# Optimization experiments

Hardware: AMD Instinct MI355X
Metric: run time of the kernel (lower is better)

Reference implementation:

```python
import jax, jax.numpy as jnp
import numpy as np

EPS = 1e-8

def setup_inputs() -> dict:
    key = jax.random.key(0)
    k = jax.random.split(key, 5)
    b, cin, cout, hw, kh = 8, 128, 128, 256, 3
    cond = 128
    return {
        "x": jax.random.normal(k[0], (b, cin, hw, hw), jnp.float32),
        "y": jax.random.normal(k[1], (b, cond), jnp.float32),
        "conv_w": jax.random.normal(k[2], (cout, cin, kh, kh), jnp.float32) * 0.05,
        "gamma_w": jax.random.normal(k[3], (cin, cond), jnp.float32) * 0.05,
        "gamma_b": jnp.zeros((cin,), jnp.float32),
    }

def reference(x, y, conv_w, gamma_w, gamma_b):
    # x: [b, cin, h, w]; y: [b, cond]; conv_w: [cout, cin, kh, kw]
    b, c, h, w = x.shape
    cout = conv_w.shape[0]
    gamma = y @ gamma_w.T + gamma_b                                   # [b, cin]  (fc_gamma)
    weight = conv_w[None] * (gamma[:, None, :, None, None] + 1.0)     # [b, cout, cin, kh, kw]
    # demodulation: rsqrt of sum of squares over (cin, kh, kw)
    d = jax.lax.rsqrt(jnp.sum(weight * weight, axis=(2, 3, 4), keepdims=True) + EPS)
    weight = weight * d
    # grouped conv with groups = batch
    xg = x.reshape(1, b * c, h, w)
    wg = weight.reshape(b * cout, c, conv_w.shape[2], conv_w.shape[3])
    out = jax.lax.conv_general_dilated(
        xg, wg, window_strides=(1, 1), padding="SAME",
        dimension_numbers=("NCHW", "OIHW", "NCHW"),
        feature_group_count=b)
    return out.reshape(b, cout, h, w)
```

## Files before the change

### kernel.cpp

```cpp
#include <hip/hip_runtime.h>

typedef _Float16 f16;
typedef _Float16 f16x8 __attribute__((ext_vector_type(8)));
typedef float f32x4 __attribute__((ext_vector_type(4)));

#define NB 8
#define NC 128
#define HW 256
#define EPSV 1e-8f

__global__ __launch_bounds__(256) void k_weights(
    const float* __restrict__ y, const float* __restrict__ conv_w,
    const float* __restrict__ gamma_w, const float* __restrict__ gamma_b,
    f16* __restrict__ W16)
{
    int b  = blockIdx.x >> 7;
    int co = blockIdx.x & 127;
    int t  = threadIdx.x;

    __shared__ float g1[128];
    __shared__ float part[256];
    __shared__ float red[256];

    {
        int ci = t & 127, hf = t >> 7;
        const float* yb = y + b * 128 + hf * 64;
        const float* gw = gamma_w + (size_t)ci * 128 + hf * 64;
        float s = 0.f;
        #pragma unroll 8
        for (int j = 0; j < 64; ++j) s += yb[j] * gw[j];
        part[t] = s;
    }
    __syncthreads();
    if (t < 128) g1[t] = part[t] + part[t + 128] + gamma_b[t] + 1.0f;
    __syncthreads();

    const float* wrow = conv_w + (size_t)co * 1152;
    float ssq = 0.f;
    for (int i = t; i < 1152; i += 256) {
        int ci = i / 9;
        float wv = wrow[i] * g1[ci];
        ssq += wv * wv;
    }
    red[t] = ssq;
    __syncthreads();
    for (int s = 128; s > 0; s >>= 1) {
        if (t < s) red[t] += red[t + s];
        __syncthreads();
    }
    float d = rsqrtf(red[0] + EPSV);

    for (int i = t; i < 1152; i += 256) {
        int ci = i / 9, tap = i - ci * 9;
        float wv = wrow[i] * g1[ci] * d;
        int chunk = ci >> 5, ci_in = ci & 31;
        size_t wi = (((size_t)((b * 9 + tap) * 4 + chunk) * 128 + co) << 5) + ci_in;
        W16[wi] = (f16)wv;
    }
}

__global__ __launch_bounds__(256) void k_transpose(
    const float* __restrict__ x, f16* __restrict__ x16)
{
    int b = blockIdx.x >> 8;
    int y = blockIdx.x & 255;
    int l = threadIdx.x;

    const float* src = x + ((size_t)b * 128 * 65536) + (size_t)y * 256 + l;

    for (int c0 = 0; c0 < 128; c0 += 8) {
        uint u[4];
        #pragma unroll
        for (int i = 0; i < 8; i += 2) {
            float v0 = src[(size_t)(c0 + i) * 65536];
            float v1 = src[(size_t)(c0 + i + 1) * 65536];
            f16 h0 = (f16)v0, h1 = (f16)v1;
            ushort u0 = *(ushort*)&h0, u1 = *(ushort*)&h1;
            u[i >> 1] = (uint)u0 | ((uint)u1 << 16);
        }
        int chunk = c0 >> 5, ci_in = c0 & 31;
        f16* dst = x16 + (((size_t)(b * 4 + chunk) * 65536 + (size_t)y * 256 + l) << 5) + ci_in;
        *(uint4*)dst = *(uint4*)u;
    }
}

__device__ __forceinline__ uint4 load_xs_g(const f16* xc, int idx, int y0, int x0)
{
    int r = idx / 72;
    int rem = idx - r * 72;
    int yy = y0 + r - 1;
    int xx = x0 + (rem >> 2) - 1;
    if ((unsigned)yy < 256u && (unsigned)xx < 256u)
        return *(const uint4*)(xc + ((((size_t)yy << 8) + xx) << 5) + ((rem & 3) << 3));
    return make_uint4(0u, 0u, 0u, 0u);
}

__global__ __launch_bounds__(256) void k_conv(
    const f16* __restrict__ x16, const f16* __restrict__ W16,
    float* __restrict__ out)
{
    int blk  = blockIdx.x;
    int tile = blk & 511;
    int b    = blk >> 9;
    int tc   = tile & 15, tr = tile >> 4;
    int y0   = tr * 8, x0 = tc * 16;

    __shared__ f16 As[2][128 * 40];
    __shared__ f16 Xs[2][180 * 32];

    int t    = threadIdx.x;
    int w    = t >> 6, lane = t & 63;
    int wm   = (w >> 1) * 64;
    int wn   = (w & 1) * 4;
    int l15  = lane & 15;
    int k8   = lane >> 4;

    const f16* Wb = W16 + (size_t)b * 147456;

    {
        const f16* xc = x16 + (size_t)(b * 4) * 2097152;
        for (int idx = t; idx < 720; idx += 256) {
            uint4 v = load_xs_g(xc, idx, y0, x0);
            *(uint4*)((char*)(&Xs[0][0]) + (size_t)idx * 16) = v;
        }
        const uint4* asrc = (const uint4*)Wb;
        uint4* adst = (uint4*)((char*)(&As[0][0]) + (t >> 1) * 80 + (t & 1) * 32);
        adst[0] = asrc[(t >> 1) * 4 + (t & 1) * 2];
        adst[1] = asrc[(t >> 1) * 4 + (t & 1) * 2 + 1];
    }
    __syncthreads();

    f32x4 acc[4][4];
    #pragma unroll
    for (int mi = 0; mi < 4; ++mi)
        #pragma unroll
        for (int nj = 0; nj < 4; ++nj)
            acc[mi][nj] = (f32x4){0.f, 0.f, 0.f, 0.f};

    int chunk = 0, tap = 0;
    for (int it = 0; it < 36; ++it) {
        bool preA = it < 35;
        bool preX = (tap == 0) && (chunk < 3);

        uint4 a0 = {}, a1 = {};
        if (preA) {
            int tn = tap + 1, cn = chunk;
            if (tn == 9) { tn = 0; cn = chunk + 1; }
            const uint4* asrc = (const uint4*)(Wb + (size_t)(tn * 4 + cn) * 4096);
            a0 = asrc[(t >> 1) * 4 + (t & 1) * 2];
            a1 = asrc[(t >> 1) * 4 + (t & 1) * 2 + 1];
        }
        uint4 xv0 = {}, xv1 = {}, xv2 = {};
        if (preX) {
            const f16* xc = x16 + (size_t)(b * 4 + chunk + 1) * 2097152;
            xv0 = load_xs_g(xc, t, y0, x0);
            xv1 = load_xs_g(xc, t + 256, y0, x0);
            if (t < 208) xv2 = load_xs_g(xc, t + 512, y0, x0);
        }

        int dy = tap / 3, dx = tap - dy * 3;
        const f16* Ab = &As[it & 1][0];
        const f16* Xb = &Xs[chunk & 1][0];

        f16x8 af[4];
        #pragma unroll
        for (int mi = 0; mi < 4; ++mi)
            af[mi] = *(const f16x8*)(Ab + (wm + mi * 16 + l15) * 40 + k8 * 8);

        f16x8 bf[4];
        #pragma unroll
        for (int nj = 0; nj < 4; ++nj) {
            int p = (wn + nj + dy) * 18 + dx + l15;
            bf[nj] = *(const f16x8*)(Xb + p * 32 + k8 * 8);
        }

        #pragma unroll
        for (int mi = 0; mi < 4; ++mi)
            #pragma unroll
            for (int nj = 0; nj < 4; ++nj)
                acc[mi][nj] = __builtin_amdgcn_mfma_f32_16x16x32_f16(
                    af[mi], bf[nj], acc[mi][nj], 0, 0, 0);

        if (preA) {
            uint4* adst = (uint4*)((char*)(&As[(it + 1) & 1][0]) + (t >> 1) * 80 + (t & 1) * 32);
            adst[0] = a0; adst[1] = a1;
        }
        if (preX) {
            char* xd = (char*)(&Xs[(chunk + 1) & 1][0]);
            *(uint4*)(xd + (size_t)t * 16) = xv0;
            *(uint4*)(xd + (size_t)(t + 256) * 16) = xv1;
            if (t < 208) *(uint4*)(xd + (size_t)(t + 512) * 16) = xv2;
        }
        __syncthreads();

        if (++tap == 9) { tap = 0; ++chunk; }
    }

    size_t obase = (size_t)b << 23;
    #pragma unroll
    for (int mi = 0; mi < 4; ++mi) {
        #pragma unroll
        for (int r = 0; r < 4; ++r) {
            int co = wm + mi * 16 + k8 * 4 + r;
            float* orow = out + obase + ((size_t)co << 16);
            #pragma unroll
            for (int nj = 0; nj < 4; ++nj) {
                int yy = y0 + wn + nj;
                orow[(size_t)yy * 256 + x0 + l15] = acc[mi][nj][r];
            }
        }
    }
}

extern "C" void kernel_launch(void* const* d_in, const int* in_sizes, int n_in,
                              void* d_out, int out_size, void* d_ws, size_t ws_size,
                              hipStream_t stream)
{
    const float* x       = (const float*)d_in[0];
    const float* y       = (const float*)d_in[1];
    const float* conv_w  = (const float*)d_in[2];
    const float* gamma_w = (const float*)d_in[3];
    const float* gamma_b = (const float*)d_in[4];
    float* out = (float*)d_out;

    f16* x16 = (f16*)d_ws;
    f16* W16 = (f16*)((char*)d_ws + 134217728ull);

    k_weights<<<dim3(1024), dim3(256), 0, stream>>>(y, conv_w, gamma_w, gamma_b, W16);
    k_transpose<<<dim3(2048), dim3(256), 0, stream>>>(x, x16);
    k_conv<<<dim3(4096), dim3(256), 0, stream>>>(x16, W16, out);
}
```

Before: 671.9 us.

## Fuse fp32-to-fp16 input conversion into conv kernel, drop transpose pass

Removes the separate transpose kernel that converted x to a channel-interleaved fp16 buffer, and instead has the conv kernel load fp32 NCHW data directly, convert to fp16 and pack into shared memory. It also changes shared-memory pitches to 72 bytes for both A and X tiles, likely to reduce bank conflicts. This saves a full write and re-read of a 128MB intermediate. In exchange, each tile's global loads become strided scalar fp32 reads (8 channels at 256KB stride), halo data is re-read across tiles, and more registers are held during prefetch.

```diff
diff --git a/kernel.cpp b/kernel.cpp
--- a/kernel.cpp
+++ b/kernel.cpp
@@ -8,6 +8,9 @@
 #define NC 128
 #define HW 256
 #define EPSV 1e-8f
+
+#define APITCH 72
+#define XPITCH 72
 
 __global__ __launch_bounds__(256) void k_weights(
     const float* __restrict__ y, const float* __restrict__ conv_w,
@@ -59,44 +62,41 @@
     }
 }
 
-__global__ __launch_bounds__(256) void k_transpose(
-    const float* __restrict__ x, f16* __restrict__ x16)
-{
-    int b = blockIdx.x >> 8;
-    int y = blockIdx.x & 255;
-    int l = threadIdx.x;
-
-    const float* src = x + ((size_t)b * 128 * 65536) + (size_t)y * 256 + l;
-
-    for (int c0 = 0; c0 < 128; c0 += 8) {
-        uint u[4];
-        #pragma unroll
-        for (int i = 0; i < 8; i += 2) {
-            float v0 = src[(size_t)(c0 + i) * 65536];
-            float v1 = src[(size_t)(c0 + i + 1) * 65536];
-            f16 h0 = (f16)v0, h1 = (f16)v1;
-            ushort u0 = *(ushort*)&h0, u1 = *(ushort*)&h1;
-            u[i >> 1] = (uint)u0 | ((uint)u1 << 16);
-        }
-        int chunk = c0 >> 5, ci_in = c0 & 31;
-        f16* dst = x16 + (((size_t)(b * 4 + chunk) * 65536 + (size_t)y * 256 + l) << 5) + ci_in;
-        *(uint4*)dst = *(uint4*)u;
-    }
-}
-
-__device__ __forceinline__ uint4 load_xs_g(const f16* xc, int idx, int y0, int x0)
-{
-    int r = idx / 72;
+
+__device__ __forceinline__ void load8(float* __restrict__ v,
+                                      const float* __restrict__ xb,
+                                      int idx, int y0, int x0)
+{
+    int r   = idx / 72;
     int rem = idx - r * 72;
-    int yy = y0 + r - 1;
-    int xx = x0 + (rem >> 2) - 1;
-    if ((unsigned)yy < 256u && (unsigned)xx < 256u)
-        return *(const uint4*)(xc + ((((size_t)yy << 8) + xx) << 5) + ((rem & 3) << 3));
-    return make_uint4(0u, 0u, 0u, 0u);
+    int yy  = y0 + r - 1;
+    int xx  = x0 + (rem >> 2) - 1;
+    if (((unsigned)yy < 256u) & ((unsigned)xx < 256u)) {
+        const float* p = xb + (((size_t)(rem & 3)) << 19) + ((yy << 8) + xx);
+        #pragma unroll
+        for (int j = 0; j < 8; ++j) v[j] = p[(size_t)j << 16];
+    } else {
+        #pragma unroll
+        for (int j = 0; j < 8; ++j) v[j] = 0.f;
+    }
+}
+
+__device__ __forceinline__ void pack_write(char* __restrict__ xdst, int idx,
+                                           const float* __restrict__ v)
+{
+    uint u[4];
+    #pragma unroll
+    for (int j = 0; j < 8; j += 2) {
+        f16 h0 = (f16)v[j], h1 = (f16)v[j + 1];
+        ushort u0 = *(const ushort*)&h0, u1 = *(const ushort*)&h1;
+        u[j >> 1] = (uint)u0 | ((uint)u1 << 16);
+    }
+    int p = idx >> 2, g = idx & 3;
+    *(uint4*)(xdst + p * XPITCH + g * 16) = *(uint4*)u;
 }
 
 __global__ __launch_bounds__(256) void k_conv(
-    const f16* __restrict__ x16, const f16* __restrict__ W16,
+    const float* __restrict__ x, const f16* __restrict__ W16,
     float* __restrict__ out)
 {
     int blk  = blockIdx.x;
@@ -105,8 +105,8 @@
     int tc   = tile & 15, tr = tile >> 4;
     int y0   = tr * 8, x0 = tc * 16;
 
-    __shared__ f16 As[2][128 * 40];
-    __shared__ f16 Xs[2][180 * 32];
+    __shared__ char As[2][128 * APITCH];
+    __shared__ char Xs[2][180 * XPITCH];
 
     int t    = threadIdx.x;
     int w    = t >> 6, lane = t & 63;
@@ -118,13 +118,14 @@
     const f16* Wb = W16 + (size_t)b * 147456;
 
     {
-        const f16* xc = x16 + (size_t)(b * 4) * 2097152;
+        const float* xb0 = x + ((size_t)(b * 128) << 16);
         for (int idx = t; idx < 720; idx += 256) {
-            uint4 v = load_xs_g(xc, idx, y0, x0);
-            *(uint4*)((char*)(&Xs[0][0]) + (size_t)idx * 16) = v;
+            float v[8];
+            load8(v, xb0, idx, y0, x0);
+            pack_write(&Xs[0][0], idx, v);
         }
         const uint4* asrc = (const uint4*)Wb;
-        uint4* adst = (uint4*)((char*)(&As[0][0]) + (t >> 1) * 80 + (t & 1) * 32);
+        uint4* adst = (uint4*)(&As[0][0] + (t >> 1) * APITCH + (t & 1) * 32);
         adst[0] = asrc[(t >> 1) * 4 + (t & 1) * 2];
         adst[1] = asrc[(t >> 1) * 4 + (t & 1) * 2 + 1];
     }
@@ -150,28 +151,28 @@
             a0 = asrc[(t >> 1) * 4 + (t & 1) * 2];
             a1 = asrc[(t >> 1) * 4 + (t & 1) * 2 + 1];
         }
-        uint4 xv0 = {}, xv1 = {}, xv2 = {};
+        float xv0[8], xv1[8], xv2[8];
         if (preX) {
-            const f16* xc = x16 + (size_t)(b * 4 + chunk + 1) * 2097152;
-            xv0 = load_xs_g(xc, t, y0, x0);
-            xv1 = load_xs_g(xc, t + 256, y0, x0);
-            if (t < 208) xv2 = load_xs_g(xc, t + 512, y0, x0);
+            const float* xbn = x + ((size_t)(b * 128 + (chunk + 1) * 32) << 16);
+            load8(xv0, xbn, t, y0, x0);
+            load8(xv1, xbn, t + 256, y0, x0);
+            if (t < 208) load8(xv2, xbn, t + 512, y0, x0);
         }
 
         int dy = tap / 3, dx = tap - dy * 3;
-        const f16* Ab = &As[it & 1][0];
-        const f16* Xb = &Xs[chunk & 1][0];
+        const char* Ab = &As[it & 1][0];
+        const char* Xb = &Xs[chunk & 1][0];
 
         f16x8 af[4];
         #pragma unroll
         for (int mi = 0; mi < 4; ++mi)
-            af[mi] = *(const f16x8*)(Ab + (wm + mi * 16 + l15) * 40 + k8 * 8);
+            af[mi] = *(const f16x8*)(Ab + (wm + mi * 16 + l15) * APITCH + k8 * 16);
 
         f16x8 bf[4];
         #pragma unroll
         for (int nj = 0; nj < 4; ++nj) {
             int p = (wn + nj + dy) * 18 + dx + l15;
-            bf[nj] = *(const f16x8*)(Xb + p * 32 + k8 * 8);
+            bf[nj] = *(const f16x8*)(Xb + p * XPITCH + k8 * 16);
         }
 
         #pragma unroll
@@ -182,14 +183,14 @@
                     af[mi], bf[nj], acc[mi][nj], 0, 0, 0);
 
         if (preA) {
-            uint4* adst = (uint4*)((char*)(&As[(it + 1) & 1][0]) + (t >> 1) * 80 + (t & 1) * 32);
+            uint4* adst = (uint4*)(&As[(it + 1) & 1][0] + (t >> 1) * APITCH + (t & 1) * 32);
             adst[0] = a0; adst[1] = a1;
         }
         if (preX) {
-            char* xd = (char*)(&Xs[(chunk + 1) & 1][0]);
-            *(uint4*)(xd + (size_t)t * 16) = xv0;
-            *(uint4*)(xd + (size_t)(t + 256) * 16) = xv1;
-            if (t < 208) *(uint4*)(xd + (size_t)(t + 512) * 16) = xv2;
+            char* xd = &Xs[(chunk + 1) & 1][0];
+            pack_write(xd, t, xv0);
+            pack_write(xd, t + 256, xv1);
+            if (t < 208) pack_write(xd, t + 512, xv2);
         }
         __syncthreads();
 
@@ -223,10 +224,8 @@
     const float* gamma_b = (const float*)d_in[4];
     float* out = (float*)d_out;
 
-    f16* x16 = (f16*)d_ws;
-    f16* W16 = (f16*)((char*)d_ws + 134217728ull);
+    f16* W16 = (f16*)d_ws;
 
     k_weights<<<dim3(1024), dim3(256), 0, stream>>>(y, conv_w, gamma_w, gamma_b, W16);
-    k_transpose<<<dim3(2048), dim3(256), 0, stream>>>(x, x16);
-    k_conv<<<dim3(4096), dim3(256), 0, stream>>>(x16, W16, out);
-}
+    k_conv<<<dim3(4096), dim3(256), 0, stream>>>(x, W16, out);
+}
```

Result: slower. 1.007 ms (+49.9%).
